# Optimization experiments

Measured on AMD Instinct MI355X. Metric: run time of the kernel, lower is better.

## Reference

```python
import jax, jax.numpy as jnp
import numpy as np

B, N, C, H = 4, 1024, 768, 12
D = C // H  # head dim = 64
SCALE = D ** -0.5


def setup_inputs() -> dict:
    key = jax.random.key(0)
    ks = jax.random.split(key, 13)
    inp = {
        'q': jax.random.normal(ks[0], (N, B, C), jnp.float32),
        'k': jax.random.normal(ks[1], (N, B, C), jnp.float32),
        'v': jax.random.normal(ks[2], (N, B, C), jnp.float32),
        'attn_mask': jax.random.randint(ks[3], (B, N), 0, 2).astype(bool),
        'Wq': jax.random.normal(ks[4], (C, C), jnp.float32) * 0.02,
        'bq': jax.random.normal(ks[5], (C,), jnp.float32) * 0.02,
        'Wk': jax.random.normal(ks[6], (C, C), jnp.float32) * 0.02,
        'bk': jax.random.normal(ks[7], (C,), jnp.float32) * 0.02,
        'Wv': jax.random.normal(ks[8], (C, C), jnp.float32) * 0.02,
        'bv': jax.random.normal(ks[9], (C,), jnp.float32) * 0.02,
        'Wo': jax.random.normal(ks[10], (C, C), jnp.float32) * 0.02,
        'bo': jax.random.normal(ks[11], (C,), jnp.float32) * 0.02,
        'zeta': jnp.ones((1, H, 1, D), jnp.float32),  # orig (1,1,H,1,D); leading 1 dropped by [0]
    }
    return inp


def reference(q, k, v, attn_mask, Wq, bq, Wk, bk, Wv, bv, Wo, bo, zeta):
    # inputs are [N, B, C]; module permutes to [B, N, C]
    q = q.transpose(1, 0, 2)
    k = k.transpose(1, 0, 2)
    v = v.transpose(1, 0, 2)
    b, n_q, c = q.shape
    n_k = k.shape[1]

    def heads(x, W, bias):
        y = x @ W.T + bias                          # [B, N, C]
        return y.reshape(b, -1, H, D).transpose(0, 2, 1, 3)  # [B, H, N, D]

    qh = heads(q, Wq, bq) * zeta
    kh = heads(k, Wk, bk) * zeta
    vh = heads(v, Wv, bv) * zeta

    scores = jnp.einsum('bhqd,bhkd->bhqk', qh, kh)
    mask_add = jnp.where(attn_mask[:, None, None, :], -jnp.inf, 0.0).astype(scores.dtype)
    # torch path: baddbmm(mask, q, k^T) * scale -> (qk + mask) * scale
    attn = jax.nn.softmax((scores + mask_add) * SCALE, axis=-1)

    x = jnp.einsum('bhqk,bhkd->bhqd', attn, vh)
    x = x.transpose(0, 2, 1, 3).reshape(b, n_q, c)  # [B, N_q, C]
    x = x @ Wo.T + bo
    return x.transpose(1, 0, 2)  # back to [N_q, B, C]
```

## Files before the change

kernel.cpp:

```cpp
#include <hip/hip_runtime.h>
#include <cstdint>
#include <cstddef>

typedef unsigned short us;
using short8 = __attribute__((ext_vector_type(8))) short;
using f32x4  = __attribute__((ext_vector_type(4))) float;

union U8 { us u[8]; short8 v; };
union PU { int w[4]; short8 v; };

#define MFMA16(a,b,c) __builtin_amdgcn_mfma_f32_16x16x32_bf16((a),(b),(c),0,0,0)

static __device__ __forceinline__ us f2bf(float f){
  union { float f; unsigned u; } cv; cv.f = f;
  unsigned u = cv.u;
  return (us)((u + 0x7fffu + ((u >> 16) & 1u)) >> 16);
}

typedef const __attribute__((address_space(1))) void* gp_t;
typedef __attribute__((address_space(3))) void* lp_t;
#define GL16(g,l) __builtin_amdgcn_global_load_lds((gp_t)(g),(lp_t)(l),16,0,0)

__global__ __launch_bounds__(256) void prep(
    const float* __restrict__ xq, const float* __restrict__ xk, const float* __restrict__ xv,
    const float* __restrict__ Wq, const float* __restrict__ Wk,
    const float* __restrict__ Wv, const float* __restrict__ Wo,
    const int* __restrict__ mask,
    us* __restrict__ xbq, us* __restrict__ xbk, us* __restrict__ xbv,
    us* __restrict__ wb, f32x4* __restrict__ zreg,
    int* __restrict__ rank, int* __restrict__ nbd)
{
  const int bid = blockIdx.x, tid = threadIdx.x;
  if (bid < 5760){
    unsigned id = bid * 256u + tid;
    const float* src; us* dst;
    if (id < 1179648u){
      unsigned z  = id / 393216u;
      unsigned rr = id - z * 393216u;
      unsigned row = rr / 96u, cc = rr - row * 96u;
      unsigned bsel = row >> 10, n = row & 1023u;
      const float* x = (z == 0) ? xq : (z == 1) ? xk : xv;
      us* xb = (z == 0) ? xbq : (z == 1) ? xbk : xbv;
      src = x  + (size_t)(n * 4u + bsel) * 768u + cc * 8u;
      dst = xb + (size_t)row * 768u + cc * 8u;
    } else {
      unsigned wi = id - 1179648u;
      unsigned z  = wi / 73728u;
      unsigned rr = wi - z * 73728u;
      const float* W = (z == 0) ? Wq : (z == 1) ? Wk : (z == 2) ? Wv : Wo;
      src = W  + (size_t)rr * 8u;
      dst = wb + (size_t)z * 589824u + rr * 8u;
    }
    f32x4 a = *(const f32x4*)src;
    f32x4 b = *(const f32x4*)(src + 4);
    U8 o;
#pragma unroll
    for (int j = 0; j < 4; ++j){ o.u[j] = f2bf(a[j]); o.u[4 + j] = f2bf(b[j]); }
    *(short8*)dst = o.v;
  } else if (bid < 8832){
    zreg[(size_t)(bid - 5760) * 256 + tid] = f32x4{};
  } else {
    const int b = bid - 8832, lane = tid & 63, w = tid >> 6;
    __shared__ int wsum[4];
    int m[4], cnt = 0;
#pragma unroll
    for (int j = 0; j < 4; ++j){
      m[j] = mask[b * 1024 + tid * 4 + j] ? 0 : 1;
      cnt += m[j];
    }
    int sc = cnt;
#pragma unroll
    for (int off = 1; off < 64; off <<= 1){
      int t = __shfl_up(sc, off, 64);
      if (lane >= off) sc += t;
    }
    if (lane == 63) wsum[w] = sc;
    __syncthreads();
    int woff = 0;
#pragma unroll
    for (int i = 0; i < 4; ++i) if (i < w) woff += wsum[i];
    const int total = wsum[0] + wsum[1] + wsum[2] + wsum[3];
    int rr = woff + sc - cnt;
#pragma unroll
    for (int j = 0; j < 4; ++j){
      rank[b * 1024 + tid * 4 + j] = m[j] ? rr : -1;
      rr += m[j];
    }
    if (tid == 0) nbd[b] = total;
  }
}

__global__ __launch_bounds__(256, 2) void qkv_gemm5(
    const us* __restrict__ xbq, const us* __restrict__ xbk, const us* __restrict__ xbv,
    const us* __restrict__ wb,
    const float* __restrict__ bq, const float* __restrict__ bk, const float* __restrict__ bv,
    const float* __restrict__ zeta, const int* __restrict__ rank,
    us* __restrict__ qh, us* __restrict__ kc, us* __restrict__ vtc)
{
  const int z = blockIdx.z;
  const us* A  = (z == 0) ? xbq : (z == 1) ? xbk : xbv;
  const us* Bw = wb + (size_t)z * 589824;
  const float* bias = (z == 0) ? bq : (z == 1) ? bk : bv;

  __shared__ __align__(16) us As[2][128 * 64];
  __shared__ __align__(16) us Bs[2][128 * 64];

  const int tid = threadIdx.x, lane = tid & 63, w = tid >> 6;
  const int wr = (w >> 1) * 64, wc = (w & 1) * 64;
  const int flat = blockIdx.x + blockIdx.y * 32;
  const int xcd = flat & 7, c = flat >> 3;
  const int mt = xcd * 4 + (c & 3);
  const int nt = c >> 2;

  f32x4 acc[4][4] = {};

  auto STAGE = [&](int kt, int buf){
#pragma unroll
    for (int p = 0; p < 4; ++p){
      int chunk = p * 256 + tid;
      int row = chunk >> 3;
      int colb = ((chunk & 7) ^ (row & 7)) * 8;
      GL16(A  + (size_t)(mt * 128 + row) * 768 + kt * 64 + colb,
           As[buf] + (p * 256 + w * 64) * 8);
      GL16(Bw + (size_t)(nt * 128 + row) * 768 + kt * 64 + colb,
           Bs[buf] + (p * 256 + w * 64) * 8);
    }
  };

  STAGE(0, 0);
  STAGE(1, 1);
  for (int kt = 0; kt < 12; ++kt){
    const int cur = kt & 1;
    if (kt < 11) asm volatile("s_waitcnt vmcnt(8)" ::: "memory");
    else         asm volatile("s_waitcnt vmcnt(0)" ::: "memory");
    __builtin_amdgcn_s_barrier();

#pragma unroll
    for (int ks = 0; ks < 2; ++ks){
      short8 af[4], bf4[4];
#pragma unroll
      for (int mf = 0; mf < 4; ++mf){
        int row = wr + mf * 16 + (lane & 15);
        int byte = (row * 128 + ks * 64 + (lane >> 4) * 16) ^ ((row & 7) << 4);
        af[mf] = *(const short8*)((const char*)As[cur] + byte);
      }
#pragma unroll
      for (int nf = 0; nf < 4; ++nf){
        int row = wc + nf * 16 + (lane & 15);
        int byte = (row * 128 + ks * 64 + (lane >> 4) * 16) ^ ((row & 7) << 4);
        bf4[nf] = *(const short8*)((const char*)Bs[cur] + byte);
      }
#pragma unroll
      for (int mf = 0; mf < 4; ++mf)
#pragma unroll
        for (int nf = 0; nf < 4; ++nf)
          acc[mf][nf] = MFMA16(af[mf], bf4[nf], acc[mf][nf]);
    }

    asm volatile("s_waitcnt lgkmcnt(0)" ::: "memory");
    __builtin_amdgcn_s_barrier();
    if (kt < 10) STAGE(kt + 2, cur);
  }

  float bzv[4], zzv[4]; int colv[4];
#pragma unroll
  for (int nf = 0; nf < 4; ++nf){
    colv[nf] = nt * 128 + wc + nf * 16 + (lane & 15);
    bzv[nf] = bias[colv[nf]];
    zzv[nf] = zeta[colv[nf]];
  }

  if (z == 0){
#pragma unroll
    for (int mf = 0; mf < 4; ++mf)
#pragma unroll
      for (int r = 0; r < 4; ++r){
        int row = mt * 128 + wr + mf * 16 + (lane >> 4) * 4 + r;
#pragma unroll
        for (int nf = 0; nf < 4; ++nf)
          qh[(size_t)row * 768 + colv[nf]] = f2bf((acc[mf][nf][r] + bzv[nf]) * zzv[nf]);
      }
  } else {
#pragma unroll
    for (int mf = 0; mf < 4; ++mf)
#pragma unroll
      for (int r = 0; r < 4; ++r){
        int row = mt * 128 + wr + mf * 16 + (lane >> 4) * 4 + r;
        int rk = rank[row];
        if (rk < 0) continue;
        int bsel = row >> 10;
        if (z == 1){
#pragma unroll
          for (int nf = 0; nf < 4; ++nf)
            kc[(size_t)(bsel * 1024 + rk) * 768 + colv[nf]] =
                f2bf((acc[mf][nf][r] + bzv[nf]) * zzv[nf]);
        } else {
#pragma unroll
          for (int nf = 0; nf < 4; ++nf){
            int hh = colv[nf] >> 6, dd = colv[nf] & 63;
            vtc[((size_t)(bsel * 12 + hh) * 64 + dd) * 1024 + rk] =
                f2bf((acc[mf][nf][r] + bzv[nf]) * zzv[nf]);
          }
        }
      }
  }
}

__global__ __launch_bounds__(256) void attn_fwd5(
    const us* __restrict__ qh, const us* __restrict__ kc,
    const us* __restrict__ vtc, const int* __restrict__ nbd,
    us* __restrict__ ao)
{
  const int flat = blockIdx.x + 16 * blockIdx.y + 192 * blockIdx.z;
  const int xcd = flat & 7, c = flat >> 3;
  const int pair = xcd * 6 + (c >> 4);
  const int qt = c & 15, h = pair % 12, b = pair / 12;
  const int tid = threadIdx.x, lane = tid & 63, w = tid >> 6;

  const int nbv = nbd[b];
  const int nt = (nbv + 63) >> 6;

  __shared__ __align__(16) us Ks[2][64 * 64];
  __shared__ __align__(16) us Vs[2][64 * 64];

  short8 qf[2];
#pragma unroll
  for (int ks = 0; ks < 2; ++ks)
    qf[ks] = *(const short8*)(qh +
              (size_t)(b * 1024 + qt * 64 + w * 16 + (lane & 15)) * 768 +
              h * 64 + ks * 32 + (lane >> 4) * 8);

  short8 kr[2], vr[2];
  auto KVLOAD = [&](int kt){
#pragma unroll
    for (int p = 0; p < 2; ++p){
      int cc = p * 256 + tid, row = cc >> 3, db = (cc & 7) * 8;
      kr[p] = *(const short8*)(kc + (size_t)(b * 1024 + kt * 64 + row) * 768 + h * 64 + db);
      vr[p] = *(const short8*)(vtc + ((size_t)((b * 12 + h) * 64 + row)) * 1024 + kt * 64 + db);
    }
  };
  auto KVWRITE = [&](int buf){
#pragma unroll
    for (int p = 0; p < 2; ++p){
      int cc = p * 256 + tid, row = cc >> 3, db = (cc & 7) * 8;
      int byte = (row * 128 + db * 2) ^ ((row & 7) << 4);
      *(short8*)((char*)Ks[buf] + byte) = kr[p];
      *(short8*)((char*)Vs[buf] + byte) = vr[p];
    }
  };
  KVLOAD(0); KVWRITE(0);
  __syncthreads();

  const int bpbase = (((lane & 16) << 1) | (lane & 15)) << 2;
  const bool hi5 = (lane & 32) != 0;

  float lsum = 0.f;
  f32x4 o[4] = {};
  int cur = 0;
  for (int kt = 0; kt < nt; ++kt){
    if (kt + 1 < nt) KVLOAD(kt + 1);

    f32x4 s[4] = {};
#pragma unroll
    for (int ks = 0; ks < 2; ++ks)
#pragma unroll
      for (int f = 0; f < 4; ++f){
        int row = f * 16 + (lane & 15);
        short8 kf = *(const short8*)((const char*)Ks[cur] +
                    ((row * 128 + ks * 64 + (lane >> 4) * 16) ^ ((row & 7) << 4)));
        s[f] = MFMA16(kf, qf[ks], s[f]);
      }

    float p_[4][4];
#pragma unroll
    for (int f = 0; f < 4; ++f)
#pragma unroll
      for (int r = 0; r < 4; ++r)
        p_[f][r] = __expf(s[f][r] * 0.125f);
    if (kt == nt - 1){
      int kb = kt * 64 + ((lane >> 4) << 2);
#pragma unroll
      for (int f = 0; f < 4; ++f)
#pragma unroll
        for (int r = 0; r < 4; ++r)
          p_[f][r] = (kb + f * 16 + r < nbv) ? p_[f][r] : 0.f;
    }
#pragma unroll
    for (int f = 0; f < 4; ++f)
      lsum += (p_[f][0] + p_[f][1]) + (p_[f][2] + p_[f][3]);

    unsigned pk[4][2];
#pragma unroll
    for (int f = 0; f < 4; ++f){
      pk[f][0] = (unsigned)f2bf(p_[f][0]) | ((unsigned)f2bf(p_[f][1]) << 16);
      pk[f][1] = (unsigned)f2bf(p_[f][2]) | ((unsigned)f2bf(p_[f][3]) << 16);
    }

    PU pa0, pa1;
#pragma unroll
    for (int j = 0; j < 4; ++j){
      int addr = bpbase + ((j & 2) << 5);
      int wsel = j & 1;
      int t0 = __builtin_amdgcn_ds_bpermute(addr, (int)pk[0][wsel]);
      int t1 = __builtin_amdgcn_ds_bpermute(addr, (int)pk[1][wsel]);
      int t2 = __builtin_amdgcn_ds_bpermute(addr, (int)pk[2][wsel]);
      int t3 = __builtin_amdgcn_ds_bpermute(addr, (int)pk[3][wsel]);
      pa0.w[j] = hi5 ? t1 : t0;
      pa1.w[j] = hi5 ? t3 : t2;
    }

#pragma unroll
    for (int df = 0; df < 4; ++df){
      int vrow = df * 16 + (lane & 15);
      short8 vb0 = *(const short8*)((const char*)Vs[cur] +
                   ((vrow * 128 + 0  + (lane >> 4) * 16) ^ ((vrow & 7) << 4)));
      short8 vb1 = *(const short8*)((const char*)Vs[cur] +
                   ((vrow * 128 + 64 + (lane >> 4) * 16) ^ ((vrow & 7) << 4)));
      o[df] = MFMA16(pa0.v, vb0, o[df]);
      o[df] = MFMA16(pa1.v, vb1, o[df]);
    }

    if (kt + 1 < nt) KVWRITE(cur ^ 1);
    __syncthreads();
    cur ^= 1;
  }

  float l = lsum;
  l += __shfl_xor(l, 16, 64);
  l += __shfl_xor(l, 32, 64);
  float linv[4];
#pragma unroll
  for (int r = 0; r < 4; ++r)
    linv[r] = __builtin_amdgcn_rcpf(__shfl(l, (lane >> 4) * 4 + r, 64));

#pragma unroll
  for (int df = 0; df < 4; ++df)
#pragma unroll
    for (int r = 0; r < 4; ++r){
      int qrow = qt * 64 + w * 16 + (lane >> 4) * 4 + r;
      int dcol = df * 16 + (lane & 15);
      ao[(size_t)(b * 1024 + qrow) * 768 + h * 64 + dcol] = f2bf(o[df][r] * linv[r]);
    }
}

__global__ __launch_bounds__(256, 2) void out_gemm4(
    const us* __restrict__ ain, const us* __restrict__ wo,
    const float* __restrict__ bo, float* __restrict__ dout)
{
  __shared__ __align__(16) us As[2][128 * 64];
  __shared__ __align__(16) us Bs[2][128 * 64];

  const int tid = threadIdx.x, lane = tid & 63, w = tid >> 6;
  const int wr = (w >> 1) * 64, wc = (w & 1) * 64;
  const int flat = blockIdx.x + blockIdx.y * 32;
  const int xcd = flat & 7, c = flat >> 3;
  const int mt = xcd * 4 + (c & 3);
  const int nt = c >> 2;

  f32x4 acc[4][4] = {};

  auto STAGE = [&](int kt, int buf){
#pragma unroll
    for (int p = 0; p < 4; ++p){
      int chunk = p * 256 + tid;
      int row = chunk >> 3;
      int colb = ((chunk & 7) ^ (row & 7)) * 8;
      GL16(ain + (size_t)(mt * 128 + row) * 768 + kt * 64 + colb,
           As[buf] + (p * 256 + w * 64) * 8);
      GL16(wo  + (size_t)(nt * 128 + row) * 768 + kt * 64 + colb,
           Bs[buf] + (p * 256 + w * 64) * 8);
    }
  };

  STAGE(0, 0);
  STAGE(1, 1);
  for (int kt = 0; kt < 12; ++kt){
    const int cur = kt & 1;
    if (kt < 11) asm volatile("s_waitcnt vmcnt(8)" ::: "memory");
    else         asm volatile("s_waitcnt vmcnt(0)" ::: "memory");
    __builtin_amdgcn_s_barrier();

#pragma unroll
    for (int ks = 0; ks < 2; ++ks){
      short8 af[4], bf4[4];
#pragma unroll
      for (int mf = 0; mf < 4; ++mf){
        int row = wr + mf * 16 + (lane & 15);
        int byte = (row * 128 + ks * 64 + (lane >> 4) * 16) ^ ((row & 7) << 4);
        af[mf] = *(const short8*)((const char*)As[cur] + byte);
      }
#pragma unroll
      for (int nf = 0; nf < 4; ++nf){
        int row = wc + nf * 16 + (lane & 15);
        int byte = (row * 128 + ks * 64 + (lane >> 4) * 16) ^ ((row & 7) << 4);
        bf4[nf] = *(const short8*)((const char*)Bs[cur] + byte);
      }
#pragma unroll
      for (int mf = 0; mf < 4; ++mf)
#pragma unroll
        for (int nf = 0; nf < 4; ++nf)
          acc[mf][nf] = MFMA16(af[mf], bf4[nf], acc[mf][nf]);
    }

    asm volatile("s_waitcnt lgkmcnt(0)" ::: "memory");
    __builtin_amdgcn_s_barrier();
    if (kt < 10) STAGE(kt + 2, cur);
  }

#pragma unroll
  for (int nf = 0; nf < 4; ++nf){
    int col = nt * 128 + wc + nf * 16 + (lane & 15);
    float bz = bo[col];
#pragma unroll
    for (int mf = 0; mf < 4; ++mf)
#pragma unroll
      for (int r = 0; r < 4; ++r){
        int row = mt * 128 + wr + mf * 16 + (lane >> 4) * 4 + r;
        int n = row & 1023, bsel = row >> 10;
        dout[(size_t)(n * 4 + bsel) * 768 + col] = acc[mf][nf][r] + bz;
      }
  }
}

extern "C" void kernel_launch(void* const* d_in, const int* in_sizes, int n_in,
                              void* d_out, int out_size, void* d_ws, size_t ws_size,
                              hipStream_t stream)
{
  const float* q    = (const float*)d_in[0];
  const float* k    = (const float*)d_in[1];
  const float* v    = (const float*)d_in[2];
  const int*   mask = (const int*)d_in[3];
  const float* Wq   = (const float*)d_in[4];
  const float* bq   = (const float*)d_in[5];
  const float* Wk   = (const float*)d_in[6];
  const float* bk   = (const float*)d_in[7];
  const float* Wv   = (const float*)d_in[8];
  const float* bv   = (const float*)d_in[9];
  const float* Wo   = (const float*)d_in[10];
  const float* bo   = (const float*)d_in[11];
  const float* zeta = (const float*)d_in[12];

  us* xbq = (us*)d_out;
  us* xbk = xbq + 3145728;
  us* xbv = (us*)d_ws;
  us* wb  = xbv + 3145728;
  us* qh  = wb  + 2359296;
  us* kc  = qh  + 3145728;
  us* vtc = kc  + 3145728;
  int* rank = (int*)(vtc + 3145728);
  int* nbd  = rank + 4096;
  us* ao = xbv;

  prep<<<8836, 256, 0, stream>>>(q, k, v, Wq, Wk, Wv, Wo, mask,
                                 xbq, xbk, xbv, wb, (f32x4*)kc, rank, nbd);
  qkv_gemm5<<<dim3(32, 6, 3), 256, 0, stream>>>(xbq, xbk, xbv, wb, bq, bk, bv,
                                                zeta, rank, qh, kc, vtc);
  attn_fwd5<<<dim3(16, 12, 4), 256, 0, stream>>>(qh, kc, vtc, nbd, ao);
  out_gemm4<<<dim3(32, 6, 1), 256, 0, stream>>>(ao, wb + 3 * 589824, bo, (float*)d_out);
}
```

Before: 80.49 us.

## Compact unmasked K/V rows before projection GEMM and skip empty tiles

Mask compaction now runs in its own small kernel ahead of prep. Prep uses the result to write only unmasked K and V rows, packing them contiguously with each batch padded to 128 rows. The K/V projection GEMM blocks then exit early when they fall past the compacted row count, so roughly half of the K/V projection work on masked keys is skipped. The cost is an extra kernel launch and serialisation before prep, and with random masks the compacted tiles of different batches no longer line up with a fixed layout.

```diff
diff --git a/kernel.cpp b/kernel.cpp
--- a/kernel.cpp
+++ b/kernel.cpp
@@ -17,87 +17,118 @@
   return (us)((u + 0x7fffu + ((u >> 16) & 1u)) >> 16);
 }
 
+static __device__ __forceinline__ int base_of(const int* nbd, int b){
+  int s = 0;
+#pragma unroll
+  for (int i = 0; i < 3; ++i) if (i < b) s += (nbd[i] + 127) & ~127;
+  return s;
+}
+
 typedef const __attribute__((address_space(1))) void* gp_t;
 typedef __attribute__((address_space(3))) void* lp_t;
 #define GL16(g,l) __builtin_amdgcn_global_load_lds((gp_t)(g),(lp_t)(l),16,0,0)
+
+__global__ __launch_bounds__(256) void compact_idx(
+    const int* __restrict__ mask, int* __restrict__ rank, int* __restrict__ nbd)
+{
+  const int b = blockIdx.x, tid = threadIdx.x, lane = tid & 63, w = tid >> 6;
+  __shared__ int wsum[4];
+
+  int m[4], cnt = 0;
+#pragma unroll
+  for (int j = 0; j < 4; ++j){
+    m[j] = mask[b * 1024 + tid * 4 + j] ? 0 : 1;
+    cnt += m[j];
+  }
+  int sc = cnt;
+#pragma unroll
+  for (int off = 1; off < 64; off <<= 1){
+    int t = __shfl_up(sc, off, 64);
+    if (lane >= off) sc += t;
+  }
+  if (lane == 63) wsum[w] = sc;
+  __syncthreads();
+  int woff = 0;
+#pragma unroll
+  for (int i = 0; i < 4; ++i) if (i < w) woff += wsum[i];
+  const int total = wsum[0] + wsum[1] + wsum[2] + wsum[3];
+  int rr = woff + sc - cnt;
+#pragma unroll
+  for (int j = 0; j < 4; ++j){
+    rank[b * 1024 + tid * 4 + j] = m[j] ? rr : -1;
+    rr += m[j];
+  }
+  if (tid == 0) nbd[b] = total;
+}
 
 __global__ __launch_bounds__(256) void prep(
     const float* __restrict__ xq, const float* __restrict__ xk, const float* __restrict__ xv,
     const float* __restrict__ Wq, const float* __restrict__ Wk,
     const float* __restrict__ Wv, const float* __restrict__ Wo,
-    const int* __restrict__ mask,
+    const int* __restrict__ rank, const int* __restrict__ nbd,
     us* __restrict__ xbq, us* __restrict__ xbk, us* __restrict__ xbv,
-    us* __restrict__ wb, f32x4* __restrict__ zreg,
-    int* __restrict__ rank, int* __restrict__ nbd)
+    us* __restrict__ wb, f32x4* __restrict__ zreg)
 {
   const int bid = blockIdx.x, tid = threadIdx.x;
-  if (bid < 5760){
-    unsigned id = bid * 256u + tid;
-    const float* src; us* dst;
-    if (id < 1179648u){
-      unsigned z  = id / 393216u;
-      unsigned rr = id - z * 393216u;
-      unsigned row = rr / 96u, cc = rr - row * 96u;
-      unsigned bsel = row >> 10, n = row & 1023u;
-      const float* x = (z == 0) ? xq : (z == 1) ? xk : xv;
-      us* xb = (z == 0) ? xbq : (z == 1) ? xbk : xbv;
+  if (bid >= 5760){
+    zreg[(size_t)(bid - 5760) * 256 + tid] = f32x4{};
+    return;
+  }
+  unsigned id = bid * 256u + tid;
+  const float* src; us* dst;
+  if (id < 1179648u){
+    unsigned z  = id / 393216u;
+    unsigned rr = id - z * 393216u;
+    unsigned row = rr / 96u, cc = rr - row * 96u;
+    unsigned bsel = row >> 10, n = row & 1023u;
+    if (z == 0){
+      src = xq  + (size_t)(n * 4u + bsel) * 768u + cc * 8u;
+      dst = xbq + (size_t)row * 768u + cc * 8u;
+    } else {
+      int rk = rank[row];
+      if (rk < 0) return;
+      int grow = base_of(nbd, (int)bsel) + rk;
+      const float* x = (z == 1) ? xk : xv;
+      us* xb = (z == 1) ? xbk : xbv;
       src = x  + (size_t)(n * 4u + bsel) * 768u + cc * 8u;
-      dst = xb + (size_t)row * 768u + cc * 8u;
-    } else {
-      unsigned wi = id - 1179648u;
-      unsigned z  = wi / 73728u;
-      unsigned rr = wi - z * 73728u;
-      const float* W = (z == 0) ? Wq : (z == 1) ? Wk : (z == 2) ? Wv : Wo;
-      src = W  + (size_t)rr * 8u;
-      dst = wb + (size_t)z * 589824u + rr * 8u;
-    }
-    f32x4 a = *(const f32x4*)src;
-    f32x4 b = *(const f32x4*)(src + 4);
-    U8 o;
-#pragma unroll
-    for (int j = 0; j < 4; ++j){ o.u[j] = f2bf(a[j]); o.u[4 + j] = f2bf(b[j]); }
-    *(short8*)dst = o.v;
-  } else if (bid < 8832){
-    zreg[(size_t)(bid - 5760) * 256 + tid] = f32x4{};
+      dst = xb + (size_t)grow * 768u + cc * 8u;
+    }
   } else {
-    const int b = bid - 8832, lane = tid & 63, w = tid >> 6;
-    __shared__ int wsum[4];
-    int m[4], cnt = 0;
-#pragma unroll
-    for (int j = 0; j < 4; ++j){
-      m[j] = mask[b * 1024 + tid * 4 + j] ? 0 : 1;
-      cnt += m[j];
-    }
-    int sc = cnt;
-#pragma unroll
-    for (int off = 1; off < 64; off <<= 1){
-      int t = __shfl_up(sc, off, 64);
-      if (lane >= off) sc += t;
-    }
-    if (lane == 63) wsum[w] = sc;
-    __syncthreads();
-    int woff = 0;
-#pragma unroll
-    for (int i = 0; i < 4; ++i) if (i < w) woff += wsum[i];
-    const int total = wsum[0] + wsum[1] + wsum[2] + wsum[3];
-    int rr = woff + sc - cnt;
-#pragma unroll
-    for (int j = 0; j < 4; ++j){
-      rank[b * 1024 + tid * 4 + j] = m[j] ? rr : -1;
-      rr += m[j];
-    }
-    if (tid == 0) nbd[b] = total;
-  }
-}
-
-__global__ __launch_bounds__(256, 2) void qkv_gemm5(
+    unsigned wi = id - 1179648u;
+    unsigned z  = wi / 73728u;
+    unsigned rr = wi - z * 73728u;
+    const float* W = (z == 0) ? Wq : (z == 1) ? Wk : (z == 2) ? Wv : Wo;
+    src = W  + (size_t)rr * 8u;
+    dst = wb + (size_t)z * 589824u + rr * 8u;
+  }
+  f32x4 a = *(const f32x4*)src;
+  f32x4 b = *(const f32x4*)(src + 4);
+  U8 o;
+#pragma unroll
+  for (int j = 0; j < 4; ++j){ o.u[j] = f2bf(a[j]); o.u[4 + j] = f2bf(b[j]); }
+  *(short8*)dst = o.v;
+}
+
+__global__ __launch_bounds__(256, 2) void qkv_gemm6(
     const us* __restrict__ xbq, const us* __restrict__ xbk, const us* __restrict__ xbv,
     const us* __restrict__ wb,
     const float* __restrict__ bq, const float* __restrict__ bk, const float* __restrict__ bv,
-    const float* __restrict__ zeta, const int* __restrict__ rank,
+    const float* __restrict__ zeta, const int* __restrict__ nbd,
     us* __restrict__ qh, us* __restrict__ kc, us* __restrict__ vtc)
 {
   const int z = blockIdx.z;
+  int mt, nt;
+  if (z == 0){
+    const int flat = blockIdx.x + blockIdx.y * 32;
+    const int xcd = flat & 7, c = flat >> 3;
+    mt = xcd * 4 + (c & 3);
+    nt = c >> 2;
+  } else {
+    mt = blockIdx.x;
+    nt = blockIdx.y;
+    const int R = base_of(nbd, 3) + ((nbd[3] + 127) & ~127);
+    if (mt * 128 >= R) return;
+  }
   const us* A  = (z == 0) ? xbq : (z == 1) ? xbk : xbv;
   const us* Bw = wb + (size_t)z * 589824;
   const float* bias = (z == 0) ? bq : (z == 1) ? bk : bv;
@@ -107,10 +138,6 @@
 
   const int tid = threadIdx.x, lane = tid & 63, w = tid >> 6;
   const int wr = (w >> 1) * 64, wc = (w & 1) * 64;
-  const int flat = blockIdx.x + blockIdx.y * 32;
-  const int xcd = flat & 7, c = flat >> 3;
-  const int mt = xcd * 4 + (c & 3);
-  const int nt = c >> 2;
 
   f32x4 acc[4][4] = {};
 
@@ -181,24 +208,28 @@
           qh[(size_t)row * 768 + colv[nf]] = f2bf((acc[mf][nf][r] + bzv[nf]) * zzv[nf]);
       }
   } else {
+    const int row0 = mt * 128;
+    const int b0 = base_of(nbd, 1), b1 = base_of(nbd, 2), b2 = base_of(nbd, 3);
+    const int bsel = (row0 >= b0) + (row0 >= b1) + (row0 >= b2);
+    const int base_b = (bsel == 0) ? 0 : (bsel == 1) ? b0 : (bsel == 2) ? b1 : b2;
+    const int nb = nbd[bsel];
 #pragma unroll
     for (int mf = 0; mf < 4; ++mf)
 #pragma unroll
       for (int r = 0; r < 4; ++r){
-        int row = mt * 128 + wr + mf * 16 + (lane >> 4) * 4 + r;
-        int rk = rank[row];
-        if (rk < 0) continue;
-        int bsel = row >> 10;
+        int grow = mt * 128 + wr + mf * 16 + (lane >> 4) * 4 + r;
+        int row_local = grow - base_b;
+        if (row_local >= nb) continue;
         if (z == 1){
 #pragma unroll
           for (int nf = 0; nf < 4; ++nf)
-            kc[(size_t)(bsel * 1024 + rk) * 768 + colv[nf]] =
+            kc[(size_t)grow * 768 + colv[nf]] =
                 f2bf((acc[mf][nf][r] + bzv[nf]) * zzv[nf]);
         } else {
 #pragma unroll
           for (int nf = 0; nf < 4; ++nf){
             int hh = colv[nf] >> 6, dd = colv[nf] & 63;
-            vtc[((size_t)(bsel * 12 + hh) * 64 + dd) * 1024 + rk] =
+            vtc[((size_t)(bsel * 12 + hh) * 64 + dd) * 1024 + row_local] =
                 f2bf((acc[mf][nf][r] + bzv[nf]) * zzv[nf]);
           }
         }
@@ -206,7 +237,7 @@
   }
 }
 
-__global__ __launch_bounds__(256) void attn_fwd5(
+__global__ __launch_bounds__(256) void attn_fwd6(
     const us* __restrict__ qh, const us* __restrict__ kc,
     const us* __restrict__ vtc, const int* __restrict__ nbd,
     us* __restrict__ ao)
@@ -218,6 +249,7 @@
   const int tid = threadIdx.x, lane = tid & 63, w = tid >> 6;
 
   const int nbv = nbd[b];
+  const int base_b = base_of(nbd, b);
   const int nt = (nbv + 63) >> 6;
 
   __shared__ __align__(16) us Ks[2][64 * 64];
@@ -235,7 +267,7 @@
 #pragma unroll
     for (int p = 0; p < 2; ++p){
       int cc = p * 256 + tid, row = cc >> 3, db = (cc & 7) * 8;
-      kr[p] = *(const short8*)(kc + (size_t)(b * 1024 + kt * 64 + row) * 768 + h * 64 + db);
+      kr[p] = *(const short8*)(kc + (size_t)(base_b + kt * 64 + row) * 768 + h * 64 + db);
       vr[p] = *(const short8*)(vtc + ((size_t)((b * 12 + h) * 64 + row)) * 1024 + kt * 64 + db);
     }
   };
@@ -451,10 +483,11 @@
   int* nbd  = rank + 4096;
   us* ao = xbv;
 
-  prep<<<8836, 256, 0, stream>>>(q, k, v, Wq, Wk, Wv, Wo, mask,
-                                 xbq, xbk, xbv, wb, (f32x4*)kc, rank, nbd);
-  qkv_gemm5<<<dim3(32, 6, 3), 256, 0, stream>>>(xbq, xbk, xbv, wb, bq, bk, bv,
-                                                zeta, rank, qh, kc, vtc);
-  attn_fwd5<<<dim3(16, 12, 4), 256, 0, stream>>>(qh, kc, vtc, nbd, ao);
+  compact_idx<<<4, 256, 0, stream>>>(mask, rank, nbd);
+  prep<<<8832, 256, 0, stream>>>(q, k, v, Wq, Wk, Wv, Wo, rank, nbd,
+                                 xbq, xbk, xbv, wb, (f32x4*)kc);
+  qkv_gemm6<<<dim3(32, 6, 3), 256, 0, stream>>>(xbq, xbk, xbv, wb, bq, bk, bv,
+                                                zeta, nbd, qh, kc, vtc);
+  attn_fwd6<<<dim3(16, 12, 4), 256, 0, stream>>>(qh, kc, vtc, nbd, ao);
   out_gemm4<<<dim3(32, 6, 1), 256, 0, stream>>>(ao, wb + 3 * 589824, bo, (float*)d_out);
 }
```

Result: slower. 86.16 us (+7.0%).
